# Optimization experiments

Hardware: AMD Instinct MI355X
Metric: run time of the kernel (lower is better)

Reference implementation:

```python
import jax, jax.numpy as jnp
from jax import lax
import numpy as np


def setup_inputs() -> dict:
    key = jax.random.key(0)
    ks = jax.random.split(key, 10)
    B, T, D, U = 2048, 200, 64, 64
    return {
        "x": jax.random.normal(ks[0], (B, T, D), dtype=jnp.float32),
        "att_scores": jax.random.uniform(ks[1], (B, T, 1), dtype=jnp.float32),
        "h0": jnp.zeros((B, U), dtype=jnp.float32),
        "w_ir": jax.random.normal(ks[2], (D, U), dtype=jnp.float32),
        "w_hr": jax.random.normal(ks[3], (U, U), dtype=jnp.float32),
        "b_ir": jax.random.normal(ks[4], (U,), dtype=jnp.float32),
        "b_hr": jax.random.normal(ks[5], (U,), dtype=jnp.float32),
        "w_ih": jax.random.normal(ks[6], (D, U), dtype=jnp.float32),
        "w_hh": jax.random.normal(ks[7], (U, U), dtype=jnp.float32),
        "b_ih": jax.random.normal(ks[8], (U,), dtype=jnp.float32),
        "b_hh": jax.random.normal(ks[9], (U,), dtype=jnp.float32),
    }


def reference(x, att_scores, h0, w_ir, w_hr, b_ir, b_hr, w_ih, w_hh, b_ih, b_hh):
    # Precompute input projections for all timesteps (one big GEMM each).
    pre_r = jnp.einsum('btd,du->btu', x, w_ir) + b_ir + b_hr  # [B,T,U]
    pre_h = jnp.einsum('btd,du->btu', x, w_ih) + b_ih          # [B,T,U]

    def step(h, inp):
        pr, ph, at = inp                                # [B,U],[B,U],[B,1]
        r = jax.nn.sigmoid(pr + h @ w_hr)               # reset gate
        h_cand = jnp.tanh(ph + r * (h @ w_hh + b_hh))   # candidate state
        h_new = (1.0 - at) * h + at * h_cand            # attention-gated update
        return h_new, h_new

    xs = (pre_r.transpose(1, 0, 2),
          pre_h.transpose(1, 0, 2),
          att_scores.transpose(1, 0, 2))                # time-major
    _, hs = lax.scan(step, h0, xs)                      # hs: [T,B,U]
    return hs.transpose(1, 0, 2)                        # [B,T,U]
```

## Files before the change

### kernel.cpp

```cpp
#include <hip/hip_runtime.h>


typedef float f32x2 __attribute__((ext_vector_type(2)));

constexpr int BATCH = 2048;
constexpr int T_STEPS = 200;
constexpr int UDIM = 64;
constexpr int NROWS = BATCH * T_STEPS;

#define STR_(x) #x
#define STR(x) STR_(x)

#define PTRLO(p) ((unsigned)(unsigned long long)(const void*)(p))
#define PTRHI(p) ((unsigned)(((unsigned long long)(const void*)(p)) >> 32))

__device__ __forceinline__ float lane_bcast(float v, int lane) {
    return __builtin_bit_cast(float, __builtin_amdgcn_readlane(__builtin_bit_cast(int, v), lane));
}
__device__ __forceinline__ float fast_sigmoid(float z) {
    return __builtin_amdgcn_rcpf(1.0f + __expf(-z));
}
__device__ __forceinline__ float fast_tanh(float z) {
    return 1.0f - 2.0f * __builtin_amdgcn_rcpf(__expf(2.0f * z) + 1.0f);
}

#define WLD(R,O) "global_load_dword v" STR(R) ", v[10:11], off offset:" STR(O) "\n\t"
#define WBUMP \
  "v_add_co_u32 v10, vcc, 0x1000, v10\n\t" \
  "v_addc_co_u32 v11, vcc, 0, v11, vcc\n\t"

#define WIN16(R0,R1,R2,R3,R4,R5,R6,R7,R8,R9,R10,R11,R12,R13,R14,R15) \
  WLD(R0,0) WLD(R1,256) WLD(R2,512) WLD(R3,768) \
  WLD(R4,1024) WLD(R5,1280) WLD(R6,1536) WLD(R7,1792) \
  WLD(R8,2048) WLD(R9,2304) WLD(R10,2560) WLD(R11,2816) \
  WLD(R12,3072) WLD(R13,3328) WLD(R14,3584) WLD(R15,3840)

#define WLOAD_A \
  WIN16(64,65,66,67,68,69,70,71,72,73,74,75,76,77,78,79) WBUMP \
  WIN16(80,81,82,83,84,85,86,87,88,89,90,91,92,93,94,95) WBUMP \
  WIN16(96,97,98,99,100,101,102,103,104,105,106,107,108,109,110,111) WBUMP \
  WIN16(112,113,114,115,116,117,118,119,120,121,122,123,124,125,126,127)

#define WLOAD_B \
  WIN16(128,129,130,131,132,133,134,135,136,137,138,139,140,141,142,143) WBUMP \
  WIN16(144,145,146,147,148,149,150,151,152,153,154,155,156,157,158,159) WBUMP \
  WIN16(160,161,162,163,164,165,166,167,168,169,170,171,172,173,174,175) WBUMP \
  WIN16(176,177,178,179,180,181,182,183,184,185,186,187,188,189,190,191)

#define LDSREADS \
  "ds_read_b128 v[192:195], v29\n\t" \
  "ds_read_b128 v[196:199], v29 offset:16\n\t" \
  "ds_read_b128 v[200:203], v29 offset:32\n\t" \
  "ds_read_b128 v[204:207], v29 offset:48\n\t" \
  "ds_read_b128 v[208:211], v29 offset:64\n\t" \
  "ds_read_b128 v[212:215], v29 offset:80\n\t" \
  "ds_read_b128 v[216:219], v29 offset:96\n\t" \
  "ds_read_b128 v[220:223], v29 offset:112\n\t" \
  "ds_read_b128 v[224:227], v29 offset:128\n\t" \
  "ds_read_b128 v[228:231], v29 offset:144\n\t" \
  "ds_read_b128 v[232:235], v29 offset:160\n\t" \
  "ds_read_b128 v[236:239], v29 offset:176\n\t" \
  "ds_read_b128 v[240:243], v29 offset:192\n\t" \
  "ds_read_b128 v[244:247], v29 offset:208\n\t" \
  "ds_read_b128 v[248:251], v29 offset:224\n\t" \
  "ds_read_b128 v[252:255], v29 offset:240\n\t"

#define PKQ(W, Q0,Q1,Q2,Q3, A0,A1,A2,A3, B0,B1,B2,B3) \
  "s_waitcnt lgkmcnt(" STR(W) ")\n\t" \
  "v_pk_fma_f32 v[32:33], v[" STR(Q0) ":" STR(Q1) "], v[" STR(A0) ":" STR(A1) "], v[32:33]\n\t" \
  "v_pk_fma_f32 v[36:37], v[" STR(Q0) ":" STR(Q1) "], v[" STR(B0) ":" STR(B1) "], v[36:37]\n\t" \
  "v_pk_fma_f32 v[34:35], v[" STR(Q2) ":" STR(Q3) "], v[" STR(A2) ":" STR(A3) "], v[34:35]\n\t" \
  "v_pk_fma_f32 v[38:39], v[" STR(Q2) ":" STR(Q3) "], v[" STR(B2) ":" STR(B3) "], v[38:39]\n\t"

#define DOTCONSUME \
  PKQ(15, 192,193,194,195,  64,65,66,67,     128,129,130,131) \
  PKQ(14, 196,197,198,199,  68,69,70,71,     132,133,134,135) \
  PKQ(13, 200,201,202,203,  72,73,74,75,     136,137,138,139) \
  PKQ(12, 204,205,206,207,  76,77,78,79,     140,141,142,143) \
  PKQ(11, 208,209,210,211,  80,81,82,83,     144,145,146,147) \
  PKQ(10, 212,213,214,215,  84,85,86,87,     148,149,150,151) \
  PKQ(9,  216,217,218,219,  88,89,90,91,     152,153,154,155) \
  PKQ(8,  220,221,222,223,  92,93,94,95,     156,157,158,159) \
  PKQ(7,  224,225,226,227,  96,97,98,99,     160,161,162,163) \
  PKQ(6,  228,229,230,231,  100,101,102,103, 164,165,166,167) \
  PKQ(5,  232,233,234,235,  104,105,106,107, 168,169,170,171) \
  PKQ(4,  236,237,238,239,  108,109,110,111, 172,173,174,175) \
  PKQ(3,  240,241,242,243,  112,113,114,115, 176,177,178,179) \
  PKQ(2,  244,245,246,247,  116,117,118,119, 180,181,182,183) \
  PKQ(1,  248,249,250,251,  120,121,122,123, 184,185,186,187) \
  PKQ(0,  252,253,254,255,  124,125,126,127, 188,189,190,191)

#define ACC_ZERO \
  "v_mov_b32 v32, 0\n\t" "v_mov_b32 v33, 0\n\t" \
  "v_mov_b32 v34, 0\n\t" "v_mov_b32 v35, 0\n\t" \
  "v_mov_b32 v36, 0\n\t" "v_mov_b32 v37, 0\n\t" \
  "v_mov_b32 v38, 0\n\t" "v_mov_b32 v39, 0\n\t"

#define ACLOBBERS \
  "v8","v9","v10","v11","v12","v13","v14","v15","v16","v17", \
  "v28","v29", \
  "v32","v33","v34","v35","v36","v37","v38","v39","v40","v41","v42","v43", \
  "v44","v45","v46","v50","v51","v52","v53", \
  "v64","v65","v66","v67","v68","v69","v70","v71", \
  "v72","v73","v74","v75","v76","v77","v78","v79", \
  "v80","v81","v82","v83","v84","v85","v86","v87", \
  "v88","v89","v90","v91","v92","v93","v94","v95", \
  "v96","v97","v98","v99","v100","v101","v102","v103", \
  "v104","v105","v106","v107","v108","v109","v110","v111", \
  "v112","v113","v114","v115","v116","v117","v118","v119", \
  "v120","v121","v122","v123","v124","v125","v126","v127", \
  "v128","v129","v130","v131","v132","v133","v134","v135", \
  "v136","v137","v138","v139","v140","v141","v142","v143", \
  "v144","v145","v146","v147","v148","v149","v150","v151", \
  "v152","v153","v154","v155","v156","v157","v158","v159", \
  "v160","v161","v162","v163","v164","v165","v166","v167", \
  "v168","v169","v170","v171","v172","v173","v174","v175", \
  "v176","v177","v178","v179","v180","v181","v182","v183", \
  "v184","v185","v186","v187","v188","v189","v190","v191", \
  "v192","v193","v194","v195","v196","v197","v198","v199", \
  "v200","v201","v202","v203","v204","v205","v206","v207", \
  "v208","v209","v210","v211","v212","v213","v214","v215", \
  "v216","v217","v218","v219","v220","v221","v222","v223", \
  "v224","v225","v226","v227","v228","v229","v230","v231", \
  "v232","v233","v234","v235","v236","v237","v238","v239", \
  "v240","v241","v242","v243","v244","v245","v246","v247", \
  "v248","v249","v250","v251","v252","v253","v254","v255", \
  "s48","s49","s50","vcc","scc","memory"

__global__ __launch_bounds__(256, 2) void rec_kernel(
    const f32x2* __restrict__ pre, const float* __restrict__ att,
    const float* __restrict__ h0,  const float* __restrict__ w_hr,
    const float* __restrict__ w_hh,const float* __restrict__ b_hh,
    float* __restrict__ out)
{
    const int u   = threadIdx.x & 63;
    const int row = (int)((blockIdx.x * blockDim.x + threadIdx.x) >> 6);

    __shared__ __align__(16) float hbuf[4][UDIM];
    const unsigned lrb = (unsigned)(unsigned long long)(&hbuf[threadIdx.x >> 6][0]);
    const unsigned lwa = lrb + 4u * (unsigned)u;

    const float* wa = w_hr + u;
    const float* wb = w_hh + u;
    const f32x2* pp = pre + (size_t)row * T_STEPS * UDIM + u;
    const float* ap = att + (size_t)row * T_STEPS;
    float*       op = out + (size_t)row * T_STEPS * UDIM + u;
    const float h0v = h0[(size_t)row * UDIM + u];
    const float bgv = b_hh[u];

    asm volatile(
        "v_mov_b32 v10, %[walo]\n\t" "v_mov_b32 v11, %[wahi]\n\t"
        WLOAD_A
        "v_mov_b32 v10, %[wblo]\n\t" "v_mov_b32 v11, %[wbhi]\n\t"
        WLOAD_B
        "v_mov_b32 v12, %[prelo]\n\t" "v_mov_b32 v13, %[prehi]\n\t"
        "v_mov_b32 v14, %[attlo]\n\t" "v_mov_b32 v15, %[atthi]\n\t"
        "v_mov_b32 v16, %[outlo]\n\t" "v_mov_b32 v17, %[outhi]\n\t"
        "v_mov_b32 v8, %[h0v]\n\t"
        "v_mov_b32 v9, %[bgv]\n\t"
        "v_mov_b32 v28, %[lwa]\n\t"
        "v_mov_b32 v29, %[lrb]\n\t"
        "global_load_dwordx2 v[40:41], v[12:13], off\n\t"
        "global_load_dword v42, v[14:15], off\n\t"
        "v_add_co_u32 v12, vcc, 0x200, v12\n\t"
        "v_addc_co_u32 v13, vcc, 0, v13, vcc\n\t"
        "v_add_co_u32 v14, vcc, 4, v14\n\t"
        "v_addc_co_u32 v15, vcc, 0, v15, vcc\n\t"
        "s_waitcnt vmcnt(0)\n\t"
        "v_mov_b32 v44, v40\n\t" "v_mov_b32 v45, v41\n\t" "v_mov_b32 v46, v42\n\t"
        "global_load_dwordx2 v[40:41], v[12:13], off\n\t"
        "global_load_dword v42, v[14:15], off\n\t"
        "v_add_co_u32 v12, vcc, 0x200, v12\n\t"
        "v_addc_co_u32 v13, vcc, 0, v13, vcc\n\t"
        "v_add_co_u32 v14, vcc, 4, v14\n\t"
        "v_addc_co_u32 v15, vcc, 0, v15, vcc\n\t"
        "ds_write_b32 v28, v8\n\t"
        "s_waitcnt lgkmcnt(0)\n\t"
        LDSREADS
        "s_movk_i32 s48, 200\n\t"
        "Lrec%=:\n\t"
        ACC_ZERO
        DOTCONSUME
        "v_add_f32 v50, v32, v33\n\t"
        "v_add_f32 v51, v34, v35\n\t"
        "v_add_f32 v52, v36, v37\n\t"
        "v_add_f32 v53, v38, v39\n\t"
        "v_add_f32 v50, v50, v51\n\t"
        "v_add_f32 v52, v52, v53\n\t"
        "v_add_f32 v50, v44, v50\n\t"
        "v_add_f32 v52, v9, v52\n\t"
        "v_mul_f32 v50, 0xbfb8aa3b, v50\n\t"
        "v_exp_f32 v50, v50\n\t"
        "s_nop 1\n\t"
        "v_add_f32 v50, 1.0, v50\n\t"
        "v_rcp_f32 v50, v50\n\t"
        "s_nop 1\n\t"
        "v_mul_f32 v52, v50, v52\n\t"
        "v_add_f32 v52, v45, v52\n\t"
        "v_mul_f32 v52, 0x4038aa3b, v52\n\t"
        "v_exp_f32 v52, v52\n\t"
        "s_nop 1\n\t"
        "v_add_f32 v52, 1.0, v52\n\t"
        "v_rcp_f32 v52, v52\n\t"
        "s_nop 1\n\t"
        "v_fma_f32 v52, -2.0, v52, 1.0\n\t"
        "v_sub_f32 v53, v52, v8\n\t"
        "v_fmac_f32 v8, v46, v53\n\t"
        "ds_write_b32 v28, v8\n\t"
        "s_waitcnt vmcnt(2)\n\t"
        "v_mov_b32 v43, v8\n\t"
        "global_store_dword v[16:17], v43, off\n\t"
        "v_add_co_u32 v16, vcc, 0x100, v16\n\t"
        "v_addc_co_u32 v17, vcc, 0, v17, vcc\n\t"
        "s_waitcnt vmcnt(1)\n\t"
        "v_mov_b32 v44, v40\n\t" "v_mov_b32 v45, v41\n\t" "v_mov_b32 v46, v42\n\t"
        "global_load_dwordx2 v[40:41], v[12:13], off\n\t"
        "global_load_dword v42, v[14:15], off\n\t"
        "s_sub_u32 s48, s48, 1\n\t"
        "s_cmp_ge_u32 s48, 3\n\t"
        "s_cselect_b32 s49, 0x200, 0\n\t"
        "s_cselect_b32 s50, 4, 0\n\t"
        "v_add_co_u32 v12, vcc, s49, v12\n\t"
        "v_addc_co_u32 v13, vcc, 0, v13, vcc\n\t"
        "v_add_co_u32 v14, vcc, s50, v14\n\t"
        "v_addc_co_u32 v15, vcc, 0, v15, vcc\n\t"
        "s_waitcnt lgkmcnt(0)\n\t"
        LDSREADS
        "s_cmp_lg_u32 s48, 0\n\t"
        "s_cbranch_scc1 Lrec%=\n\t"
        "s_waitcnt vmcnt(0) lgkmcnt(0)\n\t"
        :
        : [walo]"v"(PTRLO(wa)), [wahi]"v"(PTRHI(wa)),
          [wblo]"v"(PTRLO(wb)), [wbhi]"v"(PTRHI(wb)),
          [prelo]"v"(PTRLO(pp)), [prehi]"v"(PTRHI(pp)),
          [attlo]"v"(PTRLO(ap)), [atthi]"v"(PTRHI(ap)),
          [outlo]"v"(PTRLO(op)), [outhi]"v"(PTRHI(op)),
          [h0v]"v"(h0v), [bgv]"v"(bgv),
          [lwa]"v"(lwa), [lrb]"v"(lrb)
        : ACLOBBERS);
}

__global__ __launch_bounds__(256, 2) void proj_kernel(
    const float* __restrict__ x,  const float* __restrict__ w_ir,
    const float* __restrict__ w_ih, const float* __restrict__ b_ir,
    const float* __restrict__ b_hr, const float* __restrict__ b_ih,
    f32x2* __restrict__ pre)
{
    const int u   = threadIdx.x & 63;
    const int wid = (int)((blockIdx.x * blockDim.x + threadIdx.x) >> 6);

    __shared__ __align__(16) float xbuf[4][UDIM];
    const unsigned lrb = (unsigned)(unsigned long long)(&xbuf[threadIdx.x >> 6][0]);
    const unsigned lwa = lrb + 4u * (unsigned)u;

    const float* wa = w_ir + u;
    const float* wb = w_ih + u;
    const float* xp = x   + (size_t)wid * 100 * UDIM + u;
    f32x2*       po = pre + (size_t)wid * 100 * UDIM + u;
    const float brv = b_ir[u] + b_hr[u];
    const float bhv = b_ih[u];

    asm volatile(
        "v_mov_b32 v10, %[walo]\n\t" "v_mov_b32 v11, %[wahi]\n\t"
        WLOAD_A
        "v_mov_b32 v10, %[wblo]\n\t" "v_mov_b32 v11, %[wbhi]\n\t"
        WLOAD_B
        "v_mov_b32 v12, %[xlo]\n\t"  "v_mov_b32 v13, %[xhi]\n\t"
        "v_mov_b32 v16, %[outlo]\n\t" "v_mov_b32 v17, %[outhi]\n\t"
        "v_mov_b32 v28, %[lwa]\n\t"
        "v_mov_b32 v29, %[lrb]\n\t"
        "global_load_dword v40, v[12:13], off\n\t"
        "v_add_co_u32 v12, vcc, 0x100, v12\n\t"
        "v_addc_co_u32 v13, vcc, 0, v13, vcc\n\t"
        "s_waitcnt vmcnt(0)\n\t"
        "v_mov_b32 v44, v40\n\t"
        "global_load_dword v40, v[12:13], off\n\t"
        "v_add_co_u32 v12, vcc, 0x100, v12\n\t"
        "v_addc_co_u32 v13, vcc, 0, v13, vcc\n\t"
        "s_movk_i32 s48, 100\n\t"
        "Lproj%=:\n\t"
        "ds_write_b32 v28, v44\n\t"
        ACC_ZERO
        "s_waitcnt lgkmcnt(0)\n\t"
        LDSREADS
        DOTCONSUME
        "v_add_f32 v50, v32, v33\n\t"
        "v_add_f32 v42, v34, v35\n\t"
        "v_add_f32 v50, v50, v42\n\t"
        "v_add_f32 v51, v36, v37\n\t"
        "v_add_f32 v42, v38, v39\n\t"
        "v_add_f32 v51, v51, v42\n\t"
        "s_waitcnt vmcnt(1)\n\t"
        "v_add_f32 v52, %[brv], v50\n\t"
        "v_add_f32 v53, %[bhv], v51\n\t"
        "global_store_dwordx2 v[16:17], v[52:53], off\n\t"
        "v_add_co_u32 v16, vcc, 0x200, v16\n\t"
        "v_addc_co_u32 v17, vcc, 0, v17, vcc\n\t"
        "s_waitcnt vmcnt(1)\n\t"
        "v_mov_b32 v44, v40\n\t"
        "global_load_dword v40, v[12:13], off\n\t"
        "s_sub_u32 s48, s48, 1\n\t"
        "s_cmp_ge_u32 s48, 3\n\t"
        "s_cselect_b32 s49, 0x100, 0\n\t"
        "v_add_co_u32 v12, vcc, s49, v12\n\t"
        "v_addc_co_u32 v13, vcc, 0, v13, vcc\n\t"
        "s_cmp_lg_u32 s48, 0\n\t"
        "s_cbranch_scc1 Lproj%=\n\t"
        "s_waitcnt vmcnt(0) lgkmcnt(0)\n\t"
        :
        : [walo]"v"(PTRLO(wa)), [wahi]"v"(PTRHI(wa)),
          [wblo]"v"(PTRLO(wb)), [wbhi]"v"(PTRHI(wb)),
          [xlo]"v"(PTRLO(xp)),  [xhi]"v"(PTRHI(xp)),
          [outlo]"v"(PTRLO(po)), [outhi]"v"(PTRHI(po)),
          [brv]"v"(brv), [bhv]"v"(bhv),
          [lwa]"v"(lwa), [lrb]"v"(lrb)
        : ACLOBBERS);
}

__global__ __launch_bounds__(256) void agru_fused_kernel(
    const float* __restrict__ x, const float* __restrict__ att,
    const float* __restrict__ h0,
    const float* __restrict__ w_ir, const float* __restrict__ w_hr,
    const float* __restrict__ b_ir, const float* __restrict__ b_hr,
    const float* __restrict__ w_ih, const float* __restrict__ w_hh,
    const float* __restrict__ b_ih, const float* __restrict__ b_hh,
    float* __restrict__ out)
{
    __shared__ float lds[4 * UDIM * UDIM];
    const int tid = threadIdx.x;
    #pragma unroll
    for (int i = 0; i < 16; ++i) {
        int e = tid + 256 * i;
        lds[e] = w_ir[e]; lds[4096 + e] = w_ih[e];
        lds[8192 + e] = w_hr[e]; lds[12288 + e] = w_hh[e];
    }
    __syncthreads();

    const int wave = tid >> 6;
    const int u = tid & 63;
    const int r0 = blockIdx.x * 8 + wave * 2;
    const int r1 = r0 + 1;

    float h_0 = h0[r0 * UDIM + u];
    float h_1 = h0[r1 * UDIM + u];
    const float bR = b_ir[u] + b_hr[u];
    const float bH = b_ih[u];
    const float bG = b_hh[u];

    const float* xp0 = x + (long)r0 * T_STEPS * UDIM + u;
    const float* xp1 = x + (long)r1 * T_STEPS * UDIM + u;
    const float* ap0 = att + (long)r0 * T_STEPS;
    const float* ap1 = att + (long)r1 * T_STEPS;
    float* op0 = out + (long)r0 * T_STEPS * UDIM + u;
    float* op1 = out + (long)r1 * T_STEPS * UDIM + u;

    float xv0 = xp0[0], xv1 = xp1[0], a0 = ap0[0], a1 = ap1[0];

    for (int t = 0; t < T_STEPS; ++t) {
        const int tn = (t + 1 < T_STEPS) ? (t + 1) : t;
        float nxv0 = xp0[(long)tn * UDIM], nxv1 = xp1[(long)tn * UDIM];
        float na0 = ap0[tn], na1 = ap1[tn];

        float accR0 = bR, accR1 = bR, accH0 = bH, accH1 = bH, accG0 = bG, accG1 = bG;
        #pragma unroll
        for (int j = 0; j < 64; ++j) {
            const float wir = lds[j * 64 + u];
            const float wih = lds[4096 + j * 64 + u];
            const float whr = lds[8192 + j * 64 + u];
            const float whh = lds[12288 + j * 64 + u];
            const float xj0 = lane_bcast(xv0, j);
            const float xj1 = lane_bcast(xv1, j);
            const float hj0 = lane_bcast(h_0, j);
            const float hj1 = lane_bcast(h_1, j);
            accR0 = fmaf(xj0, wir, accR0); accR0 = fmaf(hj0, whr, accR0);
            accH0 = fmaf(xj0, wih, accH0); accG0 = fmaf(hj0, whh, accG0);
            accR1 = fmaf(xj1, wir, accR1); accR1 = fmaf(hj1, whr, accR1);
            accH1 = fmaf(xj1, wih, accH1); accG1 = fmaf(hj1, whh, accG1);
        }
        const float r0g = fast_sigmoid(accR0);
        const float r1g = fast_sigmoid(accR1);
        const float hc0 = fast_tanh(fmaf(r0g, accG0, accH0));
        const float hc1 = fast_tanh(fmaf(r1g, accG1, accH1));
        h_0 = fmaf(a0, hc0 - h_0, h_0);
        h_1 = fmaf(a1, hc1 - h_1, h_1);
        op0[(long)t * UDIM] = h_0;
        op1[(long)t * UDIM] = h_1;
        xv0 = nxv0; xv1 = nxv1; a0 = na0; a1 = na1;
    }
}

extern "C" void kernel_launch(void* const* d_in, const int* in_sizes, int n_in,
                              void* d_out, int out_size, void* d_ws, size_t ws_size,
                              hipStream_t stream) {
    (void)in_sizes; (void)n_in; (void)out_size;

    const float* x    = (const float*)d_in[0];
    const float* att  = (const float*)d_in[1];
    const float* h0   = (const float*)d_in[2];
    const float* w_ir = (const float*)d_in[3];
    const float* w_hr = (const float*)d_in[4];
    const float* b_ir = (const float*)d_in[5];
    const float* b_hr = (const float*)d_in[6];
    const float* w_ih = (const float*)d_in[7];
    const float* w_hh = (const float*)d_in[8];
    const float* b_ih = (const float*)d_in[9];
    const float* b_hh = (const float*)d_in[10];
    float* out = (float*)d_out;

    const size_t pre_bytes = (size_t)NROWS * UDIM * sizeof(f32x2);

    if (ws_size >= pre_bytes) {
        f32x2* pre = (f32x2*)d_ws;
        proj_kernel<<<dim3(1024), dim3(256), 0, stream>>>(
            x, w_ir, w_ih, b_ir, b_hr, b_ih, pre);
        rec_kernel<<<dim3(512), dim3(256), 0, stream>>>(
            pre, att, h0, w_hr, w_hh, b_hh, out);
    } else {
        agru_fused_kernel<<<dim3(256), dim3(256), 0, stream>>>(
            x, att, h0, w_ir, w_hr, b_ir, b_hr, w_ih, w_hh, b_ih, b_hh, out);
    }
}
```

Before: 267.9 us.

## Restructure projection kernel to process four rows per iteration with strided row mapping

The projection kernel now has each wave handle four consecutive x rows per iteration instead of one, with a strided mapping across the batch. It switches to scalar base addresses (SGPR + VGPR offset addressing) and issues four x loads per iteration, prefetched one iteration ahead. LDS staging grows to four rows per wave. The aim is to amortize load latency and loop overhead and raise memory-level parallelism, at the cost of dropping launch bounds to one block per SM hint and more complex addressing.

```diff
diff --git a/kernel.cpp b/kernel.cpp
--- a/kernel.cpp
+++ b/kernel.cpp
@@ -14,6 +14,9 @@
 #define PTRLO(p) ((unsigned)(unsigned long long)(const void*)(p))
 #define PTRHI(p) ((unsigned)(((unsigned long long)(const void*)(p)) >> 32))
 
+__device__ __forceinline__ unsigned rfl(unsigned x) {
+    return (unsigned)__builtin_amdgcn_readfirstlane((int)x);
+}
 __device__ __forceinline__ float lane_bcast(float v, int lane) {
     return __builtin_bit_cast(float, __builtin_amdgcn_readlane(__builtin_bit_cast(int, v), lane));
 }
@@ -24,46 +27,28 @@
     return 1.0f - 2.0f * __builtin_amdgcn_rcpf(__expf(2.0f * z) + 1.0f);
 }
 
-#define WLD(R,O) "global_load_dword v" STR(R) ", v[10:11], off offset:" STR(O) "\n\t"
-#define WBUMP \
-  "v_add_co_u32 v10, vcc, 0x1000, v10\n\t" \
-  "v_addc_co_u32 v11, vcc, 0, v11, vcc\n\t"
-
-#define WIN16(R0,R1,R2,R3,R4,R5,R6,R7,R8,R9,R10,R11,R12,R13,R14,R15) \
-  WLD(R0,0) WLD(R1,256) WLD(R2,512) WLD(R3,768) \
-  WLD(R4,1024) WLD(R5,1280) WLD(R6,1536) WLD(R7,1792) \
-  WLD(R8,2048) WLD(R9,2304) WLD(R10,2560) WLD(R11,2816) \
-  WLD(R12,3072) WLD(R13,3328) WLD(R14,3584) WLD(R15,3840)
-
-#define WLOAD_A \
-  WIN16(64,65,66,67,68,69,70,71,72,73,74,75,76,77,78,79) WBUMP \
-  WIN16(80,81,82,83,84,85,86,87,88,89,90,91,92,93,94,95) WBUMP \
-  WIN16(96,97,98,99,100,101,102,103,104,105,106,107,108,109,110,111) WBUMP \
-  WIN16(112,113,114,115,116,117,118,119,120,121,122,123,124,125,126,127)
-
-#define WLOAD_B \
-  WIN16(128,129,130,131,132,133,134,135,136,137,138,139,140,141,142,143) WBUMP \
-  WIN16(144,145,146,147,148,149,150,151,152,153,154,155,156,157,158,159) WBUMP \
-  WIN16(160,161,162,163,164,165,166,167,168,169,170,171,172,173,174,175) WBUMP \
-  WIN16(176,177,178,179,180,181,182,183,184,185,186,187,188,189,190,191)
-
-#define LDSREADS \
-  "ds_read_b128 v[192:195], v29\n\t" \
-  "ds_read_b128 v[196:199], v29 offset:16\n\t" \
-  "ds_read_b128 v[200:203], v29 offset:32\n\t" \
-  "ds_read_b128 v[204:207], v29 offset:48\n\t" \
-  "ds_read_b128 v[208:211], v29 offset:64\n\t" \
-  "ds_read_b128 v[212:215], v29 offset:80\n\t" \
-  "ds_read_b128 v[216:219], v29 offset:96\n\t" \
-  "ds_read_b128 v[220:223], v29 offset:112\n\t" \
-  "ds_read_b128 v[224:227], v29 offset:128\n\t" \
-  "ds_read_b128 v[228:231], v29 offset:144\n\t" \
-  "ds_read_b128 v[232:235], v29 offset:160\n\t" \
-  "ds_read_b128 v[236:239], v29 offset:176\n\t" \
-  "ds_read_b128 v[240:243], v29 offset:192\n\t" \
-  "ds_read_b128 v[244:247], v29 offset:208\n\t" \
-  "ds_read_b128 v[248:251], v29 offset:224\n\t" \
-  "ds_read_b128 v[252:255], v29 offset:240\n\t"
+#define LDSREADS_AT(O0,O1,O2,O3,O4,O5,O6,O7,O8,O9,O10,O11,O12,O13,O14,O15) \
+  "ds_read_b128 v[192:195], v29 offset:" STR(O0) "\n\t" \
+  "ds_read_b128 v[196:199], v29 offset:" STR(O1) "\n\t" \
+  "ds_read_b128 v[200:203], v29 offset:" STR(O2) "\n\t" \
+  "ds_read_b128 v[204:207], v29 offset:" STR(O3) "\n\t" \
+  "ds_read_b128 v[208:211], v29 offset:" STR(O4) "\n\t" \
+  "ds_read_b128 v[212:215], v29 offset:" STR(O5) "\n\t" \
+  "ds_read_b128 v[216:219], v29 offset:" STR(O6) "\n\t" \
+  "ds_read_b128 v[220:223], v29 offset:" STR(O7) "\n\t" \
+  "ds_read_b128 v[224:227], v29 offset:" STR(O8) "\n\t" \
+  "ds_read_b128 v[228:231], v29 offset:" STR(O9) "\n\t" \
+  "ds_read_b128 v[232:235], v29 offset:" STR(O10) "\n\t" \
+  "ds_read_b128 v[236:239], v29 offset:" STR(O11) "\n\t" \
+  "ds_read_b128 v[240:243], v29 offset:" STR(O12) "\n\t" \
+  "ds_read_b128 v[244:247], v29 offset:" STR(O13) "\n\t" \
+  "ds_read_b128 v[248:251], v29 offset:" STR(O14) "\n\t" \
+  "ds_read_b128 v[252:255], v29 offset:" STR(O15) "\n\t"
+
+#define LDSREADS  LDSREADS_AT(0,16,32,48,64,80,96,112,128,144,160,176,192,208,224,240)
+#define PREADS1   LDSREADS_AT(256,272,288,304,320,336,352,368,384,400,416,432,448,464,480,496)
+#define PREADS2   LDSREADS_AT(512,528,544,560,576,592,608,624,640,656,672,688,704,720,736,752)
+#define PREADS3   LDSREADS_AT(768,784,800,816,832,848,864,880,896,912,928,944,960,976,992,1008)
 
 #define PKQ(W, Q0,Q1,Q2,Q3, A0,A1,A2,A3, B0,B1,B2,B3) \
   "s_waitcnt lgkmcnt(" STR(W) ")\n\t" \
@@ -95,6 +80,58 @@
   "v_mov_b32 v34, 0\n\t" "v_mov_b32 v35, 0\n\t" \
   "v_mov_b32 v36, 0\n\t" "v_mov_b32 v37, 0\n\t" \
   "v_mov_b32 v38, 0\n\t" "v_mov_b32 v39, 0\n\t"
+
+#define WLD(R,O) "global_load_dword v" STR(R) ", v[10:11], off offset:" STR(O) "\n\t"
+#define WBUMP \
+  "v_add_co_u32 v10, vcc, 0x1000, v10\n\t" \
+  "v_addc_co_u32 v11, vcc, 0, v11, vcc\n\t"
+
+#define WIN16(R0,R1,R2,R3,R4,R5,R6,R7,R8,R9,R10,R11,R12,R13,R14,R15) \
+  WLD(R0,0) WLD(R1,256) WLD(R2,512) WLD(R3,768) \
+  WLD(R4,1024) WLD(R5,1280) WLD(R6,1536) WLD(R7,1792) \
+  WLD(R8,2048) WLD(R9,2304) WLD(R10,2560) WLD(R11,2816) \
+  WLD(R12,3072) WLD(R13,3328) WLD(R14,3584) WLD(R15,3840)
+
+#define WLOAD_A \
+  WIN16(64,65,66,67,68,69,70,71,72,73,74,75,76,77,78,79) WBUMP \
+  WIN16(80,81,82,83,84,85,86,87,88,89,90,91,92,93,94,95) WBUMP \
+  WIN16(96,97,98,99,100,101,102,103,104,105,106,107,108,109,110,111) WBUMP \
+  WIN16(112,113,114,115,116,117,118,119,120,121,122,123,124,125,126,127)
+
+#define WLOAD_B \
+  WIN16(128,129,130,131,132,133,134,135,136,137,138,139,140,141,142,143) WBUMP \
+  WIN16(144,145,146,147,148,149,150,151,152,153,154,155,156,157,158,159) WBUMP \
+  WIN16(160,161,162,163,164,165,166,167,168,169,170,171,172,173,174,175) WBUMP \
+  WIN16(176,177,178,179,180,181,182,183,184,185,186,187,188,189,190,191)
+
+#define PWLD(R,O) "global_load_dword v" STR(R) ", v14, s[56:57] offset:" STR(O) "\n\t"
+#define PWBUMP "s_add_u32 s56, s56, 0x1000\n\ts_addc_u32 s57, s57, 0\n\t"
+
+#define PWIN16(R0,R1,R2,R3,R4,R5,R6,R7,R8,R9,R10,R11,R12,R13,R14,R15) \
+  PWLD(R0,0) PWLD(R1,256) PWLD(R2,512) PWLD(R3,768) \
+  PWLD(R4,1024) PWLD(R5,1280) PWLD(R6,1536) PWLD(R7,1792) \
+  PWLD(R8,2048) PWLD(R9,2304) PWLD(R10,2560) PWLD(R11,2816) \
+  PWLD(R12,3072) PWLD(R13,3328) PWLD(R14,3584) PWLD(R15,3840)
+
+#define PWLOAD_A \
+  PWIN16(64,65,66,67,68,69,70,71,72,73,74,75,76,77,78,79) PWBUMP \
+  PWIN16(80,81,82,83,84,85,86,87,88,89,90,91,92,93,94,95) PWBUMP \
+  PWIN16(96,97,98,99,100,101,102,103,104,105,106,107,108,109,110,111) PWBUMP \
+  PWIN16(112,113,114,115,116,117,118,119,120,121,122,123,124,125,126,127)
+
+#define PWLOAD_B \
+  PWIN16(128,129,130,131,132,133,134,135,136,137,138,139,140,141,142,143) PWBUMP \
+  PWIN16(144,145,146,147,148,149,150,151,152,153,154,155,156,157,158,159) PWBUMP \
+  PWIN16(160,161,162,163,164,165,166,167,168,169,170,171,172,173,174,175) PWBUMP \
+  PWIN16(176,177,178,179,180,181,182,183,184,185,186,187,188,189,190,191)
+
+#define PREDUCE \
+  "v_add_f32 v15, v32, v33\n\t" \
+  "v_add_f32 v16, v34, v35\n\t" \
+  "v_add_f32 v15, v15, v16\n\t" \
+  "v_add_f32 v16, v36, v37\n\t" \
+  "v_add_f32 v18, v38, v39\n\t" \
+  "v_add_f32 v16, v16, v18\n\t"
 
 #define ACLOBBERS \
   "v8","v9","v10","v11","v12","v13","v14","v15","v16","v17", \
@@ -126,6 +163,37 @@
   "v240","v241","v242","v243","v244","v245","v246","v247", \
   "v248","v249","v250","v251","v252","v253","v254","v255", \
   "s48","s49","s50","vcc","scc","memory"
+
+#define PROJ_CLOBBERS \
+  "v12","v14","v15","v16","v18","v26","v27","v28","v29", \
+  "v32","v33","v34","v35","v36","v37","v38","v39", \
+  "v40","v41","v42","v43","v44","v45","v46","v47", \
+  "v48","v49","v50","v51","v52","v53","v54","v55", \
+  "v64","v65","v66","v67","v68","v69","v70","v71", \
+  "v72","v73","v74","v75","v76","v77","v78","v79", \
+  "v80","v81","v82","v83","v84","v85","v86","v87", \
+  "v88","v89","v90","v91","v92","v93","v94","v95", \
+  "v96","v97","v98","v99","v100","v101","v102","v103", \
+  "v104","v105","v106","v107","v108","v109","v110","v111", \
+  "v112","v113","v114","v115","v116","v117","v118","v119", \
+  "v120","v121","v122","v123","v124","v125","v126","v127", \
+  "v128","v129","v130","v131","v132","v133","v134","v135", \
+  "v136","v137","v138","v139","v140","v141","v142","v143", \
+  "v144","v145","v146","v147","v148","v149","v150","v151", \
+  "v152","v153","v154","v155","v156","v157","v158","v159", \
+  "v160","v161","v162","v163","v164","v165","v166","v167", \
+  "v168","v169","v170","v171","v172","v173","v174","v175", \
+  "v176","v177","v178","v179","v180","v181","v182","v183", \
+  "v184","v185","v186","v187","v188","v189","v190","v191", \
+  "v192","v193","v194","v195","v196","v197","v198","v199", \
+  "v200","v201","v202","v203","v204","v205","v206","v207", \
+  "v208","v209","v210","v211","v212","v213","v214","v215", \
+  "v216","v217","v218","v219","v220","v221","v222","v223", \
+  "v224","v225","v226","v227","v228","v229","v230","v231", \
+  "v232","v233","v234","v235","v236","v237","v238","v239", \
+  "v240","v241","v242","v243","v244","v245","v246","v247", \
+  "v248","v249","v250","v251","v252","v253","v254","v255", \
+  "s40","s41","s44","s45","s56","s57","s60","s61","vcc","scc","memory"
 
 __global__ __launch_bounds__(256, 2) void rec_kernel(
     const f32x2* __restrict__ pre, const float* __restrict__ att,
@@ -240,7 +308,7 @@
         : ACLOBBERS);
 }
 
-__global__ __launch_bounds__(256, 2) void proj_kernel(
+__global__ __launch_bounds__(256, 1) void proj_kernel(
     const float* __restrict__ x,  const float* __restrict__ w_ir,
     const float* __restrict__ w_ih, const float* __restrict__ b_ir,
     const float* __restrict__ b_hr, const float* __restrict__ b_ih,
@@ -249,72 +317,103 @@
     const int u   = threadIdx.x & 63;
     const int wid = (int)((blockIdx.x * blockDim.x + threadIdx.x) >> 6);
 
-    __shared__ __align__(16) float xbuf[4][UDIM];
-    const unsigned lrb = (unsigned)(unsigned long long)(&xbuf[threadIdx.x >> 6][0]);
+    __shared__ __align__(16) float xbuf[4][4][UDIM];
+    const unsigned lrb = (unsigned)(unsigned long long)(&xbuf[threadIdx.x >> 6][0][0]);
     const unsigned lwa = lrb + 4u * (unsigned)u;
 
-    const float* wa = w_ir + u;
-    const float* wb = w_ih + u;
-    const float* xp = x   + (size_t)wid * 100 * UDIM + u;
-    f32x2*       po = pre + (size_t)wid * 100 * UDIM + u;
+    const float* xb = x   + (size_t)wid * 4 * UDIM;
+    f32x2*       pb = pre + (size_t)wid * 4 * UDIM;
+
+    const unsigned xlo = rfl(PTRLO(xb)), xhi = rfl(PTRHI(xb));
+    const unsigned plo = rfl(PTRLO(pb)), phi = rfl(PTRHI(pb));
+    const unsigned wirlo = rfl(PTRLO(w_ir)), wirhi = rfl(PTRHI(w_ir));
+    const unsigned wihlo = rfl(PTRLO(w_ih)), wihhi = rfl(PTRHI(w_ih));
     const float brv = b_ir[u] + b_hr[u];
     const float bhv = b_ih[u];
 
     asm volatile(
-        "v_mov_b32 v10, %[walo]\n\t" "v_mov_b32 v11, %[wahi]\n\t"
-        WLOAD_A
-        "v_mov_b32 v10, %[wblo]\n\t" "v_mov_b32 v11, %[wbhi]\n\t"
-        WLOAD_B
-        "v_mov_b32 v12, %[xlo]\n\t"  "v_mov_b32 v13, %[xhi]\n\t"
-        "v_mov_b32 v16, %[outlo]\n\t" "v_mov_b32 v17, %[outhi]\n\t"
+        "s_mov_b32 s40, %[xlo]\n\t" "s_mov_b32 s41, %[xhi]\n\t"
+        "s_mov_b32 s44, %[plo]\n\t" "s_mov_b32 s45, %[phi]\n\t"
         "v_mov_b32 v28, %[lwa]\n\t"
         "v_mov_b32 v29, %[lrb]\n\t"
-        "global_load_dword v40, v[12:13], off\n\t"
-        "v_add_co_u32 v12, vcc, 0x100, v12\n\t"
-        "v_addc_co_u32 v13, vcc, 0, v13, vcc\n\t"
+        "v_sub_u32 v14, v28, v29\n\t"
+        "v_lshlrev_b32 v12, 1, v14\n\t"
+        "v_mov_b32 v26, %[brv]\n\t"
+        "v_mov_b32 v27, %[bhv]\n\t"
+        "s_mov_b32 s56, %[wirlo]\n\t" "s_mov_b32 s57, %[wirhi]\n\t"
+        PWLOAD_A
+        "s_mov_b32 s56, %[wihlo]\n\t" "s_mov_b32 s57, %[wihhi]\n\t"
+        PWLOAD_B
+        "global_load_dword v40, v14, s[40:41]\n\t"
+        "global_load_dword v41, v14, s[40:41] offset:256\n\t"
+        "global_load_dword v42, v14, s[40:41] offset:512\n\t"
+        "global_load_dword v43, v14, s[40:41] offset:768\n\t"
+        "s_add_u32 s40, s40, 0x400000\n\t" "s_addc_u32 s41, s41, 0\n\t"
         "s_waitcnt vmcnt(0)\n\t"
-        "v_mov_b32 v44, v40\n\t"
-        "global_load_dword v40, v[12:13], off\n\t"
-        "v_add_co_u32 v12, vcc, 0x100, v12\n\t"
-        "v_addc_co_u32 v13, vcc, 0, v13, vcc\n\t"
-        "s_movk_i32 s48, 100\n\t"
+        "v_mov_b32 v44, v40\n\t" "v_mov_b32 v45, v41\n\t"
+        "v_mov_b32 v46, v42\n\t" "v_mov_b32 v47, v43\n\t"
+        "s_movk_i32 s60, 25\n\t"
         "Lproj%=:\n\t"
         "ds_write_b32 v28, v44\n\t"
-        ACC_ZERO
+        "ds_write_b32 v28, v45 offset:256\n\t"
+        "ds_write_b32 v28, v46 offset:512\n\t"
+        "ds_write_b32 v28, v47 offset:768\n\t"
+        "global_load_dword v40, v14, s[40:41]\n\t"
+        "global_load_dword v41, v14, s[40:41] offset:256\n\t"
+        "global_load_dword v42, v14, s[40:41] offset:512\n\t"
+        "global_load_dword v43, v14, s[40:41] offset:768\n\t"
         "s_waitcnt lgkmcnt(0)\n\t"
         LDSREADS
+        ACC_ZERO
         DOTCONSUME
-        "v_add_f32 v50, v32, v33\n\t"
-        "v_add_f32 v42, v34, v35\n\t"
-        "v_add_f32 v50, v50, v42\n\t"
-        "v_add_f32 v51, v36, v37\n\t"
-        "v_add_f32 v42, v38, v39\n\t"
-        "v_add_f32 v51, v51, v42\n\t"
-        "s_waitcnt vmcnt(1)\n\t"
-        "v_add_f32 v52, %[brv], v50\n\t"
-        "v_add_f32 v53, %[bhv], v51\n\t"
-        "global_store_dwordx2 v[16:17], v[52:53], off\n\t"
-        "v_add_co_u32 v16, vcc, 0x200, v16\n\t"
-        "v_addc_co_u32 v17, vcc, 0, v17, vcc\n\t"
-        "s_waitcnt vmcnt(1)\n\t"
-        "v_mov_b32 v44, v40\n\t"
-        "global_load_dword v40, v[12:13], off\n\t"
-        "s_sub_u32 s48, s48, 1\n\t"
-        "s_cmp_ge_u32 s48, 3\n\t"
-        "s_cselect_b32 s49, 0x100, 0\n\t"
-        "v_add_co_u32 v12, vcc, s49, v12\n\t"
-        "v_addc_co_u32 v13, vcc, 0, v13, vcc\n\t"
-        "s_cmp_lg_u32 s48, 0\n\t"
+        PREADS1
+        PREDUCE
+        ACC_ZERO
+        "s_waitcnt vmcnt(7)\n\t"
+        "v_add_f32 v48, v26, v15\n\t"
+        "v_add_f32 v49, v27, v16\n\t"
+        "global_store_dwordx2 v12, v[48:49], s[44:45]\n\t"
+        DOTCONSUME
+        PREADS2
+        PREDUCE
+        ACC_ZERO
+        "s_waitcnt vmcnt(7)\n\t"
+        "v_add_f32 v50, v26, v15\n\t"
+        "v_add_f32 v51, v27, v16\n\t"
+        "global_store_dwordx2 v12, v[50:51], s[44:45] offset:512\n\t"
+        DOTCONSUME
+        PREADS3
+        PREDUCE
+        ACC_ZERO
+        "s_waitcnt vmcnt(7)\n\t"
+        "v_add_f32 v52, v26, v15\n\t"
+        "v_add_f32 v53, v27, v16\n\t"
+        "global_store_dwordx2 v12, v[52:53], s[44:45] offset:1024\n\t"
+        DOTCONSUME
+        PREDUCE
+        "s_waitcnt vmcnt(7)\n\t"
+        "v_add_f32 v54, v26, v15\n\t"
+        "v_add_f32 v55, v27, v16\n\t"
+        "global_store_dwordx2 v12, v[54:55], s[44:45] offset:1536\n\t"
+        "s_sub_u32 s60, s60, 1\n\t"
+        "s_cmp_ge_u32 s60, 2\n\t"
+        "s_cselect_b32 s61, 0x400000, 0\n\t"
+        "s_add_u32 s40, s40, s61\n\t" "s_addc_u32 s41, s41, 0\n\t"
+        "s_add_u32 s44, s44, 0x800000\n\t" "s_addc_u32 s45, s45, 0\n\t"
+        "s_waitcnt vmcnt(4)\n\t"
+        "v_mov_b32 v44, v40\n\t" "v_mov_b32 v45, v41\n\t"
+        "v_mov_b32 v46, v42\n\t" "v_mov_b32 v47, v43\n\t"
+        "s_cmp_lg_u32 s60, 0\n\t"
         "s_cbranch_scc1 Lproj%=\n\t"
         "s_waitcnt vmcnt(0) lgkmcnt(0)\n\t"
         :
-        : [walo]"v"(PTRLO(wa)), [wahi]"v"(PTRHI(wa)),
-          [wblo]"v"(PTRLO(wb)), [wbhi]"v"(PTRHI(wb)),
-          [xlo]"v"(PTRLO(xp)),  [xhi]"v"(PTRHI(xp)),
-          [outlo]"v"(PTRLO(po)), [outhi]"v"(PTRHI(po)),
+        : [xlo]"s"(xlo), [xhi]"s"(xhi),
+          [plo]"s"(plo), [phi]"s"(phi),
+          [wirlo]"s"(wirlo), [wirhi]"s"(wirhi),
+          [wihlo]"s"(wihlo), [wihhi]"s"(wihhi),
           [brv]"v"(brv), [bhv]"v"(bhv),
           [lwa]"v"(lwa), [lrb]"v"(lrb)
-        : ACLOBBERS);
+        : PROJ_CLOBBERS);
 }
 
 __global__ __launch_bounds__(256) void agru_fused_kernel(
```

New measurement: 236.2 us. 1.13x faster.
